# Performance work log

Measured on AMD Instinct MI355X. Metric: run time of the kernel, lower is better.

The kernel has to match this reference:

```python
import jax, jax.numpy as jnp
import numpy as np

B, S, H = 2, 2048, 1024
E_DYN, E_FIX = 8, 1
I_DYN, I_FIX = 512, 2048
TOP_K = 4
TOP_P = 0.75
JITTER_EPS = 0.1
CAPACITY_FACTOR = 1.25
MIN_CAPACITY = 4


def setup_inputs() -> dict:
    key = jax.random.key(0)
    k = jax.random.split(key, 8)
    sc = 0.02
    return {
        "hidden_states": jax.random.normal(k[0], (B, S, H), jnp.float32),
        "gate_w": jax.random.normal(k[1], (E_DYN + E_FIX, H), jnp.float32) * sc,
        "dyn_gate_w": jax.random.normal(k[2], (E_DYN, I_DYN, H), jnp.float32) * sc,
        "dyn_up_w": jax.random.normal(k[3], (E_DYN, I_DYN, H), jnp.float32) * sc,
        "dyn_down_w": jax.random.normal(k[4], (E_DYN, H, I_DYN), jnp.float32) * sc,
        "sh_gate_w": jax.random.normal(k[5], (E_FIX, I_FIX, H), jnp.float32) * sc,
        "sh_up_w": jax.random.normal(k[6], (E_FIX, I_FIX, H), jnp.float32) * sc,
        "sh_down_w": jax.random.normal(k[7], (E_FIX, H, I_FIX), jnp.float32) * sc,
    }


def _sparse_mixer(scores):
    # Inference path of audio_sparse_expert_mixer (training=False: no gumbel noise).
    T = scores.shape[0]
    rows = jnp.arange(T)
    masked_scores = scores
    mults, sels = [], []
    for _ in range(TOP_K):  # small fixed structural loop
        thr = jnp.max(masked_scores, axis=-1, keepdims=True)          # [T,1]
        sel = jnp.argmax(masked_scores, axis=-1)                       # [T]
        factor = jnp.maximum(jnp.abs(scores), jnp.abs(thr))
        jmask = (thr - scores) / factor > 2.0 * JITTER_EPS             # bool, no grad
        gates = jax.nn.softmax(jnp.where(jmask, -jnp.inf, masked_scores), axis=-1)
        mult = jnp.take_along_axis(gates, sel[:, None], axis=-1)[:, 0]
        masked_scores = masked_scores.at[rows, sel].set(-jnp.inf)
        mults.append(mult)
        sels.append(sel)
    return jnp.stack(mults, axis=-1), jnp.stack(sels, axis=-1)        # [T,K]


def reference(hidden_states, gate_w, dyn_gate_w, dyn_up_w, dyn_down_w, sh_gate_w, sh_up_w, sh_down_w):
    Bv, Sv, Hv = hidden_states.shape
    T = Bv * Sv
    x = hidden_states.reshape(T, Hv)
    full_logits = x @ gate_w.T                                         # [T, E_DYN+E_FIX]
    dyn_logits = full_logits[:, :E_DYN]

    # audio_dynamic_expert_selection: per-token dynamic expert count via top_p
    probs = jax.nn.softmax(dyn_logits, axis=-1)
    sorted_p = jnp.sort(probs, axis=-1)[:, ::-1]
    csum = jnp.cumsum(sorted_p, axis=-1)
    dyn_k = jnp.minimum(jnp.sum(csum < TOP_P, axis=-1) + 1, TOP_K)     # [T]

    mult, sel = _sparse_mixer(dyn_logits)                              # [T,K]
    slot_valid = jnp.arange(TOP_K)[None, :] < dyn_k[:, None]
    mult = jnp.where(slot_valid, mult, 0.0)

    # dense per-expert routing weights (scatter top-k multipliers, normalize)
    rows = jnp.arange(T)
    rw = jnp.zeros((T, E_DYN), x.dtype).at[rows[:, None], sel].add(mult)
    rw = rw / jnp.sum(rw, axis=-1, keepdims=True)

    # capacity-based expert dropping (_audio_expert_capacity)
    mask_dyn = (rw > 0).astype(jnp.int32)
    cap = max(int(np.ceil(T / E_DYN * CAPACITY_FACTOR)), MIN_CAPACITY)
    mask_dyn = mask_dyn * (jnp.cumsum(mask_dyn, axis=0) <= cap)
    expert_mask = jnp.concatenate([mask_dyn, jnp.ones((T, E_FIX), jnp.int32)], axis=-1)
    maskf = expert_mask.astype(x.dtype)

    # calculate_audio_global_routing_weight + router_weight * expert_mask
    gw = jax.nn.softmax(jnp.where(expert_mask == 0, -jnp.inf, full_logits), axis=-1)
    gd = rw * jnp.sum(gw[:, :E_DYN], axis=-1, keepdims=True)
    global_w = jnp.concatenate([gd, gw[:, E_DYN:]], axis=-1) * maskf   # [T, E_DYN+E_FIX]

    # dynamic experts (SwiGLU), dense reference over all experts; mask/weights zero out drops
    g = jnp.einsum('th,eih->tei', x, dyn_gate_w)
    u = jnp.einsum('th,eih->tei', x, dyn_up_w)
    y_dyn = jnp.einsum('tei,ehi->teh', jax.nn.silu(g) * u, dyn_down_w)
    out = jnp.einsum('te,teh->th', global_w[:, :E_DYN], y_dyn)

    # shared (fixed) experts applied to all tokens
    gs = jnp.einsum('th,fih->tfi', x, sh_gate_w)
    us = jnp.einsum('th,fih->tfi', x, sh_up_w)
    y_sh = jnp.einsum('tfi,fhi->tfh', jax.nn.silu(gs) * us, sh_down_w)
    out = out + jnp.einsum('tf,tfh->th', global_w[:, E_DYN:], y_sh)

    return out.reshape(Bv, Sv, Hv)
```

## Files before the change

kernel.cpp:

```cpp
#include <hip/hip_runtime.h>
#include <cstdint>

typedef __attribute__((ext_vector_type(8))) __bf16 bf16x8;
typedef __attribute__((ext_vector_type(4))) float f32x4;

static constexpr int T_TOK = 4096;
static constexpr int HDIM  = 1024;
static constexpr int NEXP  = 9;
static constexpr int EDYN  = 8;
static constexpr int IDYN_ = 512;
static constexpr int IFIX_ = 2048;
static constexpr int CAPE  = 640;

__device__ __forceinline__ unsigned short f2bf(float f) {
  unsigned u = __float_as_uint(f);
  u += 0x7fffu + ((u >> 16) & 1u);
  return (unsigned short)(u >> 16);
}

__device__ __forceinline__ void gl_lds16(const void* g, void* l) {
  __builtin_amdgcn_global_load_lds((const __attribute__((address_space(1))) void*)g,
                                   (__attribute__((address_space(3))) void*)l,
                                   16, 0, 0);
}

__global__ void cvt_kernel(const float4* __restrict__ src, ushort4* __restrict__ dst, int n4) {
  int stride = gridDim.x * blockDim.x;
  for (int i = blockIdx.x * blockDim.x + threadIdx.x; i < n4; i += stride) {
    float4 f = src[i];
    dst[i] = make_ushort4(f2bf(f.x), f2bf(f.y), f2bf(f.z), f2bf(f.w));
  }
}

__global__ __launch_bounds__(256)
void logits_kernel(const float* __restrict__ x, const float* __restrict__ gw,
                   float* __restrict__ logits) {
  int wave = threadIdx.x >> 6, lane = threadIdx.x & 63;
  int t = blockIdx.x * 4 + wave;
  if (t >= T_TOK) return;
  const float* xr = x + (size_t)t * HDIM;
  float acc[NEXP];
#pragma unroll
  for (int e = 0; e < NEXP; ++e) acc[e] = 0.f;
  for (int h = lane; h < HDIM; h += 64) {
    float xv = xr[h];
#pragma unroll
    for (int e = 0; e < NEXP; ++e) acc[e] += xv * gw[e * HDIM + h];
  }
#pragma unroll
  for (int e = 0; e < NEXP; ++e) {
    float v = acc[e];
#pragma unroll
    for (int off = 32; off > 0; off >>= 1) v += __shfl_down(v, off, 64);
    if (lane == 0) logits[t * NEXP + e] = v;
  }
}

__global__ __launch_bounds__(256)
void routing_kernel(const float* __restrict__ logits, float* __restrict__ rw,
                    int* __restrict__ mask) {
  int t = blockIdx.x * blockDim.x + threadIdx.x;
  if (t >= T_TOK) return;
  float s[EDYN];
#pragma unroll
  for (int e = 0; e < EDYN; ++e) s[e] = logits[t * NEXP + e];

  float m = s[0];
#pragma unroll
  for (int e = 1; e < EDYN; ++e) m = fmaxf(m, s[e]);
  float p[EDYN]; float psum = 0.f;
#pragma unroll
  for (int e = 0; e < EDYN; ++e) { p[e] = expf(s[e] - m); psum += p[e]; }
#pragma unroll
  for (int e = 0; e < EDYN; ++e) p[e] /= psum;
  float sp[EDYN];
#pragma unroll
  for (int e = 0; e < EDYN; ++e) sp[e] = p[e];
  for (int i = 1; i < EDYN; ++i) {
    float key = sp[i]; int j = i - 1;
    while (j >= 0 && sp[j] < key) { sp[j + 1] = sp[j]; --j; }
    sp[j + 1] = key;
  }
  float c = 0.f; int cnt = 0;
#pragma unroll
  for (int e = 0; e < EDYN; ++e) { c += sp[e]; cnt += (c < 0.75f) ? 1 : 0; }
  int dyn_k = cnt + 1; if (dyn_k > 4) dyn_k = 4;

  float ms[EDYN];
#pragma unroll
  for (int e = 0; e < EDYN; ++e) ms[e] = s[e];
  float mult[4]; int sel[4];
  for (int k = 0; k < 4; ++k) {
    float thr = ms[0]; int am = 0;
#pragma unroll
    for (int e = 1; e < EDYN; ++e) if (ms[e] > thr) { thr = ms[e]; am = e; }
    float vals[EDYN]; float mx = -INFINITY;
#pragma unroll
    for (int e = 0; e < EDYN; ++e) {
      float factor = fmaxf(fabsf(s[e]), fabsf(thr));
      float ratio = (thr - s[e]) / factor;
      float v = (ratio > 0.2f) ? -INFINITY : ms[e];
      vals[e] = v; mx = fmaxf(mx, v);
    }
    float sum = 0.f;
#pragma unroll
    for (int e = 0; e < EDYN; ++e) sum += expf(vals[e] - mx);
    mult[k] = expf(vals[am] - mx) / sum;
    sel[k] = am;
    ms[am] = -INFINITY;
  }
  float r[EDYN];
#pragma unroll
  for (int e = 0; e < EDYN; ++e) r[e] = 0.f;
  for (int k = 0; k < 4; ++k) if (k < dyn_k) r[sel[k]] += mult[k];
  float ssum = 0.f;
#pragma unroll
  for (int e = 0; e < EDYN; ++e) ssum += r[e];
#pragma unroll
  for (int e = 0; e < EDYN; ++e) {
    float v = r[e] / ssum;
    rw[t * EDYN + e] = v;
    mask[t * EDYN + e] = (v > 0.f) ? 1 : 0;
  }
}

__global__ void capacity_kernel(int* __restrict__ mask, int* __restrict__ tok,
                                int* __restrict__ counts) {
  int e = threadIdx.x >> 6;
  int lane = threadIdx.x & 63;
  int base = 0;
  for (int cIt = 0; cIt < T_TOK / 64; ++cIt) {
    int t = cIt * 64 + lane;
    int bit = mask[t * EDYN + e] != 0;
    unsigned long long bal = __ballot(bit);
    int prefix = __popcll(bal & ((1ull << lane) - 1ull));
    int cum = base + prefix + 1;
    int keep = bit && (cum <= CAPE);
    if (keep) tok[e * CAPE + (cum - 1)] = t;
    mask[t * EDYN + e] = keep;
    base += __popcll(bal);
  }
  int cnt = base < CAPE ? base : CAPE;
  if (lane == 0) counts[e] = cnt;
  for (int r = cnt + lane; r < CAPE; r += 64) tok[e * CAPE + r] = 0;
}

__global__ __launch_bounds__(256)
void final_gate_kernel(const float* __restrict__ logits, const int* __restrict__ mask,
                       const float* __restrict__ rw, float* __restrict__ gdyn,
                       float* __restrict__ wsh) {
  int t = blockIdx.x * blockDim.x + threadIdx.x;
  if (t >= T_TOK) return;
  float vals[NEXP]; float mx = -INFINITY;
  int mk[EDYN];
#pragma unroll
  for (int e = 0; e < EDYN; ++e) {
    mk[e] = mask[t * EDYN + e];
    vals[e] = mk[e] ? logits[t * NEXP + e] : -INFINITY;
    mx = fmaxf(mx, vals[e]);
  }
  vals[EDYN] = logits[t * NEXP + EDYN];
  mx = fmaxf(mx, vals[EDYN]);
  float ex[NEXP]; float sum = 0.f;
#pragma unroll
  for (int e = 0; e < NEXP; ++e) { ex[e] = expf(vals[e] - mx); sum += ex[e]; }
  float inv = 1.f / sum;
  float sd = 0.f;
#pragma unroll
  for (int e = 0; e < EDYN; ++e) sd += ex[e] * inv;
#pragma unroll
  for (int e = 0; e < EDYN; ++e)
    gdyn[t * EDYN + e] = mk[e] ? rw[t * EDYN + e] * sd : 0.f;
  wsh[t] = ex[EDYN] * inv;
}

__global__ void fill_wlist_kernel(const int* __restrict__ tok, const int* __restrict__ counts,
                                  const float* __restrict__ gdyn, float* __restrict__ wlist) {
  int i = blockIdx.x * blockDim.x + threadIdx.x;
  if (i >= EDYN * CAPE) return;
  int e = i / CAPE, r = i % CAPE;
  wlist[i] = (r < counts[e]) ? gdyn[tok[i] * EDYN + e] : 0.f;
}

template <bool GATHER>
__global__ __launch_bounds__(256)
void gemm_gateup_kernel(const unsigned short* __restrict__ xb,
                        const unsigned short* __restrict__ Wg,
                        const unsigned short* __restrict__ Wu,
                        unsigned short* __restrict__ act,
                        const int* __restrict__ toklist,
                        const int* __restrict__ counts,
                        int N, int K, int Mstride) {
  const int e = blockIdx.z;
  const int m0 = blockIdx.x * 128;
  const int n0 = blockIdx.y * 64;
  if (GATHER) { if (m0 >= counts[e]) return; }

  const unsigned short* Wg_e = Wg + (size_t)e * N * K;
  const unsigned short* Wu_e = Wu + (size_t)e * N * K;
  unsigned short* act_e = act + (size_t)e * Mstride * N;
  const int* tok_e = toklist + e * CAPE;

  __shared__ __align__(16) unsigned short As[128 * 64];
  __shared__ __align__(16) unsigned short Bgs[64 * 64];
  __shared__ __align__(16) unsigned short Bus[64 * 64];

  const int tid = threadIdx.x;
  const int lane = tid & 63;
  const int wave = tid >> 6;
  const int wr = wave >> 1, wc = wave & 1;
  const int srow = tid >> 3;
  const int scol = (tid & 7) * 8;

  const unsigned short* a_src[4];
#pragma unroll
  for (int it = 0; it < 4; ++it) {
    int r = m0 + it * 32 + srow;
    int ridx = GATHER ? tok_e[r] : r;
    a_src[it] = xb + (size_t)ridx * K + scol;
  }
  const unsigned short* bg_src[2]; const unsigned short* bu_src[2];
#pragma unroll
  for (int it = 0; it < 2; ++it) {
    int r = n0 + it * 32 + srow;
    bg_src[it] = Wg_e + (size_t)r * K + scol;
    bu_src[it] = Wu_e + (size_t)r * K + scol;
  }

  f32x4 accg[4][2], accu[4][2];
#pragma unroll
  for (int i = 0; i < 4; ++i)
#pragma unroll
    for (int j = 0; j < 2; ++j) {
      f32x4 z = {0.f, 0.f, 0.f, 0.f};
      accg[i][j] = z; accu[i][j] = z;
    }

  for (int kt = 0; kt < K; kt += 64) {
#pragma unroll
    for (int it = 0; it < 4; ++it)
      gl_lds16(a_src[it] + kt, &As[it * 2048 + wave * 512]);
#pragma unroll
    for (int it = 0; it < 2; ++it) {
      gl_lds16(bg_src[it] + kt, &Bgs[it * 2048 + wave * 512]);
      gl_lds16(bu_src[it] + kt, &Bus[it * 2048 + wave * 512]);
    }
    __syncthreads();
#pragma unroll
    for (int kk = 0; kk < 2; ++kk) {
      const int ko = kk * 32 + (lane >> 4) * 8;
      bf16x8 a[4], bg[2], bu[2];
#pragma unroll
      for (int mi = 0; mi < 4; ++mi)
        a[mi] = *reinterpret_cast<const bf16x8*>(&As[(wr * 64 + mi * 16 + (lane & 15)) * 64 + ko]);
#pragma unroll
      for (int ni = 0; ni < 2; ++ni) {
        bg[ni] = *reinterpret_cast<const bf16x8*>(&Bgs[(wc * 32 + ni * 16 + (lane & 15)) * 64 + ko]);
        bu[ni] = *reinterpret_cast<const bf16x8*>(&Bus[(wc * 32 + ni * 16 + (lane & 15)) * 64 + ko]);
      }
#pragma unroll
      for (int mi = 0; mi < 4; ++mi)
#pragma unroll
        for (int ni = 0; ni < 2; ++ni) {
          accg[mi][ni] = __builtin_amdgcn_mfma_f32_16x16x32_bf16(a[mi], bg[ni], accg[mi][ni], 0, 0, 0);
          accu[mi][ni] = __builtin_amdgcn_mfma_f32_16x16x32_bf16(a[mi], bu[ni], accu[mi][ni], 0, 0, 0);
        }
    }
    __syncthreads();
  }

#pragma unroll
  for (int mi = 0; mi < 4; ++mi)
#pragma unroll
    for (int ni = 0; ni < 2; ++ni)
#pragma unroll
      for (int j = 0; j < 4; ++j) {
        int row = m0 + wr * 64 + mi * 16 + (lane >> 4) * 4 + j;
        int col = n0 + wc * 32 + ni * 16 + (lane & 15);
        float g = accg[mi][ni][j], u = accu[mi][ni][j];
        float v = (g / (1.f + __expf(-g))) * u;
        act_e[(size_t)row * N + col] = f2bf(v);
      }
}

template <bool DYN>
__global__ __launch_bounds__(256)
void gemm_down_kernel(const unsigned short* __restrict__ act,
                      const unsigned short* __restrict__ Wd,
                      float* __restrict__ out,
                      const int* __restrict__ toklist,
                      const int* __restrict__ counts,
                      const float* __restrict__ wlist,
                      const float* __restrict__ wsh,
                      int N, int K, int Mstride) {
  const int e = blockIdx.z;
  const int m0 = blockIdx.x * 128;
  const int n0 = blockIdx.y * 128;
  if (DYN) { if (m0 >= counts[e]) return; }

  const unsigned short* A_e = act + (size_t)e * Mstride * K;
  const unsigned short* Wd_e = Wd + (size_t)e * N * K;

  __shared__ __align__(16) unsigned short As[128 * 64];
  __shared__ __align__(16) unsigned short Bs[128 * 64];

  const int tid = threadIdx.x;
  const int lane = tid & 63;
  const int wave = tid >> 6;
  const int wr = wave >> 1, wc = wave & 1;
  const int srow = tid >> 3;
  const int scol = (tid & 7) * 8;

  const unsigned short* a_src[4]; const unsigned short* b_src[4];
#pragma unroll
  for (int it = 0; it < 4; ++it) {
    a_src[it] = A_e + (size_t)(m0 + it * 32 + srow) * K + scol;
    b_src[it] = Wd_e + (size_t)(n0 + it * 32 + srow) * K + scol;
  }

  f32x4 acc[4][4];
#pragma unroll
  for (int i = 0; i < 4; ++i)
#pragma unroll
    for (int j = 0; j < 4; ++j) { f32x4 z = {0.f, 0.f, 0.f, 0.f}; acc[i][j] = z; }

  for (int kt = 0; kt < K; kt += 64) {
#pragma unroll
    for (int it = 0; it < 4; ++it) {
      gl_lds16(a_src[it] + kt, &As[it * 2048 + wave * 512]);
      gl_lds16(b_src[it] + kt, &Bs[it * 2048 + wave * 512]);
    }
    __syncthreads();
#pragma unroll
    for (int kk = 0; kk < 2; ++kk) {
      const int ko = kk * 32 + (lane >> 4) * 8;
      bf16x8 a[4], b[4];
#pragma unroll
      for (int mi = 0; mi < 4; ++mi)
        a[mi] = *reinterpret_cast<const bf16x8*>(&As[(wr * 64 + mi * 16 + (lane & 15)) * 64 + ko]);
#pragma unroll
      for (int ni = 0; ni < 4; ++ni)
        b[ni] = *reinterpret_cast<const bf16x8*>(&Bs[(wc * 64 + ni * 16 + (lane & 15)) * 64 + ko]);
#pragma unroll
      for (int mi = 0; mi < 4; ++mi)
#pragma unroll
        for (int ni = 0; ni < 4; ++ni)
          acc[mi][ni] = __builtin_amdgcn_mfma_f32_16x16x32_bf16(a[mi], b[ni], acc[mi][ni], 0, 0, 0);
    }
    __syncthreads();
  }

#pragma unroll
  for (int mi = 0; mi < 4; ++mi)
#pragma unroll
    for (int ni = 0; ni < 4; ++ni)
#pragma unroll
      for (int j = 0; j < 4; ++j) {
        int row = m0 + wr * 64 + mi * 16 + (lane >> 4) * 4 + j;
        int col = n0 + wc * 64 + ni * 16 + (lane & 15);
        float v = acc[mi][ni][j];
        if (DYN) {
          float w = wlist[e * CAPE + row];
          if (w != 0.f)
            atomicAdd(&out[(size_t)toklist[e * CAPE + row] * HDIM + col], w * v);
        } else {
          out[(size_t)row * HDIM + col] = wsh[row] * v;
        }
      }
}

extern "C" void kernel_launch(void* const* d_in, const int* in_sizes, int n_in,
                              void* d_out, int out_size, void* d_ws, size_t ws_size,
                              hipStream_t stream) {
  const float* x   = (const float*)d_in[0];
  const float* gw  = (const float*)d_in[1];
  const float* wdg = (const float*)d_in[2];
  const float* wdu = (const float*)d_in[3];
  const float* wdd = (const float*)d_in[4];
  const float* wsg = (const float*)d_in[5];
  const float* wsu = (const float*)d_in[6];
  const float* wsd = (const float*)d_in[7];
  float* out = (float*)d_out;

  char* p = (char*)d_ws;
  auto alloc = [&](size_t bytes) {
    char* r = p; p += (bytes + 255) & ~(size_t)255; return r;
  };
  unsigned short* xb    = (unsigned short*)alloc((size_t)T_TOK * HDIM * 2);
  unsigned short* wdgb  = (unsigned short*)alloc((size_t)EDYN * IDYN_ * HDIM * 2);
  unsigned short* wdub  = (unsigned short*)alloc((size_t)EDYN * IDYN_ * HDIM * 2);
  unsigned short* wddb  = (unsigned short*)alloc((size_t)EDYN * HDIM * IDYN_ * 2);
  unsigned short* wsgb  = (unsigned short*)alloc((size_t)IFIX_ * HDIM * 2);
  unsigned short* wsub  = (unsigned short*)alloc((size_t)IFIX_ * HDIM * 2);
  unsigned short* wsdb  = (unsigned short*)alloc((size_t)HDIM * IFIX_ * 2);
  unsigned short* actsh = (unsigned short*)alloc((size_t)T_TOK * IFIX_ * 2);
  unsigned short* actdy = (unsigned short*)alloc((size_t)EDYN * CAPE * IDYN_ * 2);
  float* logits = (float*)alloc((size_t)T_TOK * NEXP * 4);
  float* rw     = (float*)alloc((size_t)T_TOK * EDYN * 4);
  int*   mask   = (int*)alloc((size_t)T_TOK * EDYN * 4);
  float* gdyn   = (float*)alloc((size_t)T_TOK * EDYN * 4);
  float* wshv   = (float*)alloc((size_t)T_TOK * 4);
  int*   counts = (int*)alloc(256);
  int*   tok    = (int*)alloc((size_t)EDYN * CAPE * 4);
  float* wlist  = (float*)alloc((size_t)EDYN * CAPE * 4);

  auto cvt = [&](const float* s, unsigned short* d, size_t n) {
    int n4 = (int)(n / 4);
    int blocks = (n4 + 255) / 256; if (blocks > 2048) blocks = 2048;
    cvt_kernel<<<dim3(blocks), dim3(256), 0, stream>>>((const float4*)s, (ushort4*)d, n4);
  };
  cvt(x,   xb,   (size_t)T_TOK * HDIM);
  cvt(wdg, wdgb, (size_t)EDYN * IDYN_ * HDIM);
  cvt(wdu, wdub, (size_t)EDYN * IDYN_ * HDIM);
  cvt(wdd, wddb, (size_t)EDYN * HDIM * IDYN_);
  cvt(wsg, wsgb, (size_t)IFIX_ * HDIM);
  cvt(wsu, wsub, (size_t)IFIX_ * HDIM);
  cvt(wsd, wsdb, (size_t)HDIM * IFIX_);

  logits_kernel<<<dim3(T_TOK / 4), dim3(256), 0, stream>>>(x, gw, logits);
  routing_kernel<<<dim3(T_TOK / 256), dim3(256), 0, stream>>>(logits, rw, mask);
  capacity_kernel<<<dim3(1), dim3(512), 0, stream>>>(mask, tok, counts);
  final_gate_kernel<<<dim3(T_TOK / 256), dim3(256), 0, stream>>>(logits, mask, rw, gdyn, wshv);
  fill_wlist_kernel<<<dim3((EDYN * CAPE) / 256), dim3(256), 0, stream>>>(tok, counts, gdyn, wlist);

  gemm_gateup_kernel<false><<<dim3(T_TOK / 128, IFIX_ / 64, 1), dim3(256), 0, stream>>>(
      xb, wsgb, wsub, actsh, tok, counts, IFIX_, HDIM, T_TOK);
  gemm_down_kernel<false><<<dim3(T_TOK / 128, HDIM / 128, 1), dim3(256), 0, stream>>>(
      actsh, wsdb, out, tok, counts, wlist, wshv, HDIM, IFIX_, T_TOK);
  gemm_gateup_kernel<true><<<dim3(CAPE / 128, IDYN_ / 64, EDYN), dim3(256), 0, stream>>>(
      xb, wdgb, wdub, actdy, tok, counts, IDYN_, HDIM, CAPE);
  gemm_down_kernel<true><<<dim3(CAPE / 128, HDIM / 128, EDYN), dim3(256), 0, stream>>>(
      actdy, wddb, out, tok, counts, wlist, wshv, HDIM, IDYN_, CAPE);
}
```

Baseline: 358.1 us.

## Fuse conversions and routing kernels, parallelize capacity scan, add XCD swizzle

Merges the seven fp32-to-bf16 conversion launches into one kernel, fuses the logits and routing kernels, and rewrites the capacity scan as a per-expert block-wide prefix sum instead of one serial 512-thread block. It drops the wlist kernel by reading gdyn directly in the down-GEMM epilogue, using -1 token sentinels. It also flattens the GEMM grids and applies an XCD-aware block swizzle to the shared-expert GEMMs to improve L2 locality. These changes mainly cut launch count and serial routing time; the swizzle assumes the grid size is divisible by 8.

```diff
diff --git a/kernel.cpp b/kernel.cpp
--- a/kernel.cpp
+++ b/kernel.cpp
@@ -24,17 +24,45 @@
                                    16, 0, 0);
 }
 
-__global__ void cvt_kernel(const float4* __restrict__ src, ushort4* __restrict__ dst, int n4) {
+__device__ __forceinline__ int xcd_swz(int lin, int nwg) {
+  int q = nwg >> 3;
+  return (lin & 7) * q + (lin >> 3);
+}
+
+static constexpr int C0 = 1048576;
+static constexpr int C1 = C0 + 1048576;
+static constexpr int C2 = C1 + 1048576;
+static constexpr int C3 = C2 + 1048576;
+static constexpr int C4 = C3 + 524288;
+static constexpr int C5 = C4 + 524288;
+static constexpr int C6 = C5 + 524288;
+__global__ void cvt_all_kernel(const float4* __restrict__ s0, const float4* __restrict__ s1,
+                               const float4* __restrict__ s2, const float4* __restrict__ s3,
+                               const float4* __restrict__ s4, const float4* __restrict__ s5,
+                               const float4* __restrict__ s6,
+                               ushort4* __restrict__ d0, ushort4* __restrict__ d1,
+                               ushort4* __restrict__ d2, ushort4* __restrict__ d3,
+                               ushort4* __restrict__ d4, ushort4* __restrict__ d5,
+                               ushort4* __restrict__ d6) {
   int stride = gridDim.x * blockDim.x;
-  for (int i = blockIdx.x * blockDim.x + threadIdx.x; i < n4; i += stride) {
-    float4 f = src[i];
-    dst[i] = make_ushort4(f2bf(f.x), f2bf(f.y), f2bf(f.z), f2bf(f.w));
+  for (int i = blockIdx.x * blockDim.x + threadIdx.x; i < C6; i += stride) {
+    const float4* s; ushort4* d; int off;
+    if      (i < C0) { s = s0; d = d0; off = i; }
+    else if (i < C1) { s = s1; d = d1; off = i - C0; }
+    else if (i < C2) { s = s2; d = d2; off = i - C1; }
+    else if (i < C3) { s = s3; d = d3; off = i - C2; }
+    else if (i < C4) { s = s4; d = d4; off = i - C3; }
+    else if (i < C5) { s = s5; d = d5; off = i - C4; }
+    else             { s = s6; d = d6; off = i - C5; }
+    float4 f = s[off];
+    d[off] = make_ushort4(f2bf(f.x), f2bf(f.y), f2bf(f.z), f2bf(f.w));
   }
 }
 
 __global__ __launch_bounds__(256)
-void logits_kernel(const float* __restrict__ x, const float* __restrict__ gw,
-                   float* __restrict__ logits) {
+void logits_routing_kernel(const float* __restrict__ x, const float* __restrict__ gw,
+                           float* __restrict__ logits, float* __restrict__ rw,
+                           int* __restrict__ mask) {
   int wave = threadIdx.x >> 6, lane = threadIdx.x & 63;
   int t = blockIdx.x * 4 + wave;
   if (t >= T_TOK) return;
@@ -52,18 +80,14 @@
     float v = acc[e];
 #pragma unroll
     for (int off = 32; off > 0; off >>= 1) v += __shfl_down(v, off, 64);
-    if (lane == 0) logits[t * NEXP + e] = v;
-  }
-}
-
-__global__ __launch_bounds__(256)
-void routing_kernel(const float* __restrict__ logits, float* __restrict__ rw,
-                    int* __restrict__ mask) {
-  int t = blockIdx.x * blockDim.x + threadIdx.x;
-  if (t >= T_TOK) return;
+    acc[e] = v;
+  }
+  if (lane != 0) return;
   float s[EDYN];
 #pragma unroll
-  for (int e = 0; e < EDYN; ++e) s[e] = logits[t * NEXP + e];
+  for (int e = 0; e < NEXP; ++e) logits[t * NEXP + e] = acc[e];
+#pragma unroll
+  for (int e = 0; e < EDYN; ++e) s[e] = acc[e];
 
   float m = s[0];
 #pragma unroll
@@ -124,25 +148,40 @@
   }
 }
 
-__global__ void capacity_kernel(int* __restrict__ mask, int* __restrict__ tok,
-                                int* __restrict__ counts) {
-  int e = threadIdx.x >> 6;
-  int lane = threadIdx.x & 63;
-  int base = 0;
-  for (int cIt = 0; cIt < T_TOK / 64; ++cIt) {
-    int t = cIt * 64 + lane;
-    int bit = mask[t * EDYN + e] != 0;
-    unsigned long long bal = __ballot(bit);
-    int prefix = __popcll(bal & ((1ull << lane) - 1ull));
-    int cum = base + prefix + 1;
-    int keep = bit && (cum <= CAPE);
-    if (keep) tok[e * CAPE + (cum - 1)] = t;
-    mask[t * EDYN + e] = keep;
-    base += __popcll(bal);
-  }
-  int cnt = base < CAPE ? base : CAPE;
-  if (lane == 0) counts[e] = cnt;
-  for (int r = cnt + lane; r < CAPE; r += 64) tok[e * CAPE + r] = 0;
+__global__ __launch_bounds__(1024)
+void capacity_kernel(int* __restrict__ mask, int* __restrict__ tok,
+                     int* __restrict__ counts) {
+  const int e = blockIdx.x;
+  const int tid = threadIdx.x;
+  const int lane = tid & 63, wave = tid >> 6;
+  __shared__ int wsum[16];
+  const int t0 = tid * 4;
+  int bits[4]; int c = 0;
+#pragma unroll
+  for (int j = 0; j < 4; ++j) { bits[j] = mask[(t0 + j) * EDYN + e]; c += bits[j]; }
+  int sc = c;
+#pragma unroll
+  for (int off = 1; off < 64; off <<= 1) {
+    int v = __shfl_up(sc, off, 64);
+    if (lane >= off) sc += v;
+  }
+  if (lane == 63) wsum[wave] = sc;
+  __syncthreads();
+  int wbase = 0;
+  for (int w = 0; w < wave; ++w) wbase += wsum[w];
+  int pos = wbase + sc - c;
+#pragma unroll
+  for (int j = 0; j < 4; ++j) {
+    int keep = bits[j] && (pos < CAPE);
+    if (keep) tok[e * CAPE + pos] = t0 + j;
+    mask[(t0 + j) * EDYN + e] = keep;
+    pos += bits[j];
+  }
+  int total = 0;
+  for (int w = 0; w < 16; ++w) total += wsum[w];
+  int cnt = total < CAPE ? total : CAPE;
+  if (tid == 0) counts[e] = cnt;
+  for (int r = cnt + tid; r < CAPE; r += 1024) tok[e * CAPE + r] = -1;
 }
 
 __global__ __launch_bounds__(256)
@@ -174,14 +213,6 @@
   wsh[t] = ex[EDYN] * inv;
 }
 
-__global__ void fill_wlist_kernel(const int* __restrict__ tok, const int* __restrict__ counts,
-                                  const float* __restrict__ gdyn, float* __restrict__ wlist) {
-  int i = blockIdx.x * blockDim.x + threadIdx.x;
-  if (i >= EDYN * CAPE) return;
-  int e = i / CAPE, r = i % CAPE;
-  wlist[i] = (r < counts[e]) ? gdyn[tok[i] * EDYN + e] : 0.f;
-}
-
 template <bool GATHER>
 __global__ __launch_bounds__(256)
 void gemm_gateup_kernel(const unsigned short* __restrict__ xb,
@@ -190,10 +221,12 @@
                         unsigned short* __restrict__ act,
                         const int* __restrict__ toklist,
                         const int* __restrict__ counts,
-                        int N, int K, int Mstride) {
+                        int N, int K, int Mstride, int MT) {
   const int e = blockIdx.z;
-  const int m0 = blockIdx.x * 128;
-  const int n0 = blockIdx.y * 64;
+  int nid = blockIdx.x;
+  if (!GATHER) nid = xcd_swz(nid, gridDim.x);
+  const int m0 = (nid % MT) * 128;
+  const int n0 = (nid / MT) * 64;
   if (GATHER) { if (m0 >= counts[e]) return; }
 
   const unsigned short* Wg_e = Wg + (size_t)e * N * K;
@@ -216,7 +249,8 @@
 #pragma unroll
   for (int it = 0; it < 4; ++it) {
     int r = m0 + it * 32 + srow;
-    int ridx = GATHER ? tok_e[r] : r;
+    int ridx = r;
+    if (GATHER) { int tv = tok_e[r]; ridx = tv < 0 ? 0 : tv; }
     a_src[it] = xb + (size_t)ridx * K + scol;
   }
   const unsigned short* bg_src[2]; const unsigned short* bu_src[2];
@@ -290,12 +324,14 @@
                       float* __restrict__ out,
                       const int* __restrict__ toklist,
                       const int* __restrict__ counts,
-                      const float* __restrict__ wlist,
+                      const float* __restrict__ gdyn,
                       const float* __restrict__ wsh,
-                      int N, int K, int Mstride) {
+                      int N, int K, int Mstride, int MT) {
   const int e = blockIdx.z;
-  const int m0 = blockIdx.x * 128;
-  const int n0 = blockIdx.y * 128;
+  int nid = blockIdx.x;
+  if (!DYN) nid = xcd_swz(nid, gridDim.x);
+  const int m0 = (nid % MT) * 128;
+  const int n0 = (nid / MT) * 128;
   if (DYN) { if (m0 >= counts[e]) return; }
 
   const unsigned short* A_e = act + (size_t)e * Mstride * K;
@@ -360,9 +396,9 @@
         int col = n0 + wc * 64 + ni * 16 + (lane & 15);
         float v = acc[mi][ni][j];
         if (DYN) {
-          float w = wlist[e * CAPE + row];
-          if (w != 0.f)
-            atomicAdd(&out[(size_t)toklist[e * CAPE + row] * HDIM + col], w * v);
+          int t = toklist[e * CAPE + row];
+          if (t >= 0)
+            atomicAdd(&out[(size_t)t * HDIM + col], gdyn[t * EDYN + e] * v);
         } else {
           out[(size_t)row * HDIM + col] = wsh[row] * v;
         }
@@ -402,33 +438,23 @@
   float* wshv   = (float*)alloc((size_t)T_TOK * 4);
   int*   counts = (int*)alloc(256);
   int*   tok    = (int*)alloc((size_t)EDYN * CAPE * 4);
-  float* wlist  = (float*)alloc((size_t)EDYN * CAPE * 4);
-
-  auto cvt = [&](const float* s, unsigned short* d, size_t n) {
-    int n4 = (int)(n / 4);
-    int blocks = (n4 + 255) / 256; if (blocks > 2048) blocks = 2048;
-    cvt_kernel<<<dim3(blocks), dim3(256), 0, stream>>>((const float4*)s, (ushort4*)d, n4);
-  };
-  cvt(x,   xb,   (size_t)T_TOK * HDIM);
-  cvt(wdg, wdgb, (size_t)EDYN * IDYN_ * HDIM);
-  cvt(wdu, wdub, (size_t)EDYN * IDYN_ * HDIM);
-  cvt(wdd, wddb, (size_t)EDYN * HDIM * IDYN_);
-  cvt(wsg, wsgb, (size_t)IFIX_ * HDIM);
-  cvt(wsu, wsub, (size_t)IFIX_ * HDIM);
-  cvt(wsd, wsdb, (size_t)HDIM * IFIX_);
-
-  logits_kernel<<<dim3(T_TOK / 4), dim3(256), 0, stream>>>(x, gw, logits);
-  routing_kernel<<<dim3(T_TOK / 256), dim3(256), 0, stream>>>(logits, rw, mask);
-  capacity_kernel<<<dim3(1), dim3(512), 0, stream>>>(mask, tok, counts);
+
+  cvt_all_kernel<<<dim3(2048), dim3(256), 0, stream>>>(
+      (const float4*)x, (const float4*)wdg, (const float4*)wdu, (const float4*)wdd,
+      (const float4*)wsg, (const float4*)wsu, (const float4*)wsd,
+      (ushort4*)xb, (ushort4*)wdgb, (ushort4*)wdub, (ushort4*)wddb,
+      (ushort4*)wsgb, (ushort4*)wsub, (ushort4*)wsdb);
+
+  logits_routing_kernel<<<dim3(T_TOK / 4), dim3(256), 0, stream>>>(x, gw, logits, rw, mask);
+  capacity_kernel<<<dim3(EDYN), dim3(1024), 0, stream>>>(mask, tok, counts);
   final_gate_kernel<<<dim3(T_TOK / 256), dim3(256), 0, stream>>>(logits, mask, rw, gdyn, wshv);
-  fill_wlist_kernel<<<dim3((EDYN * CAPE) / 256), dim3(256), 0, stream>>>(tok, counts, gdyn, wlist);
-
-  gemm_gateup_kernel<false><<<dim3(T_TOK / 128, IFIX_ / 64, 1), dim3(256), 0, stream>>>(
-      xb, wsgb, wsub, actsh, tok, counts, IFIX_, HDIM, T_TOK);
-  gemm_down_kernel<false><<<dim3(T_TOK / 128, HDIM / 128, 1), dim3(256), 0, stream>>>(
-      actsh, wsdb, out, tok, counts, wlist, wshv, HDIM, IFIX_, T_TOK);
-  gemm_gateup_kernel<true><<<dim3(CAPE / 128, IDYN_ / 64, EDYN), dim3(256), 0, stream>>>(
-      xb, wdgb, wdub, actdy, tok, counts, IDYN_, HDIM, CAPE);
-  gemm_down_kernel<true><<<dim3(CAPE / 128, HDIM / 128, EDYN), dim3(256), 0, stream>>>(
-      actdy, wddb, out, tok, counts, wlist, wshv, HDIM, IDYN_, CAPE);
-}
+
+  gemm_gateup_kernel<false><<<dim3((T_TOK / 128) * (IFIX_ / 64), 1, 1), dim3(256), 0, stream>>>(
+      xb, wsgb, wsub, actsh, tok, counts, IFIX_, HDIM, T_TOK, T_TOK / 128);
+  gemm_down_kernel<false><<<dim3((T_TOK / 128) * (HDIM / 128), 1, 1), dim3(256), 0, stream>>>(
+      actsh, wsdb, out, tok, counts, gdyn, wshv, HDIM, IFIX_, T_TOK, T_TOK / 128);
+  gemm_gateup_kernel<true><<<dim3((CAPE / 128) * (IDYN_ / 64), 1, EDYN), dim3(256), 0, stream>>>(
+      xb, wdgb, wdub, actdy, tok, counts, IDYN_, HDIM, CAPE, CAPE / 128);
+  gemm_down_kernel<true><<<dim3((CAPE / 128) * (HDIM / 128), 1, EDYN), dim3(256), 0, stream>>>(
+      actdy, wddb, out, tok, counts, gdyn, wshv, HDIM, IDYN_, CAPE, CAPE / 128);
+}
```

After: 348.1 us. 1.03x faster.
